# Performance work log

Hardware: AMD Instinct MI355X
Metric: run time of the kernel (lower is better)

The kernel has to match this reference:

```python
import jax, jax.numpy as jnp
import numpy as np


def setup_inputs() -> dict:
    key = jax.random.key(0)
    k1, k2, k3, k4 = jax.random.split(key, 4)
    Q, S, L, F, H = 32, 25, 64, 256, 64
    qs = jax.random.normal(k1, (Q, L, F), dtype=jnp.float32)
    hs = jax.random.normal(k2, (S, L, F), dtype=jnp.float32)
    # nn.Linear(feature_size, hidden_size): weight [H, F], bias [H]
    W = jax.random.normal(k3, (H, F), dtype=jnp.float32) * (1.0 / np.sqrt(F))
    b = jax.random.normal(k4, (H,), dtype=jnp.float32) * 0.01
    return {"qs": qs, "hs": hs, "W": W, "b": b}


def reference(qs, hs, W, b):
    # Project once instead of materializing the repeated 5D tensors before Linear.
    # Wq: [Q, L, H], Wh: [S, L, H]
    Wq = jnp.einsum("qlf,hf->qlh", qs, W) + b
    Wh = jnp.einsum("slf,hf->slh", hs, W) + b
    # score[q,s,i,j] = sum_h tanh(Wq[q,i,h] * Wh[s,j,h])  -- non-decomposable,
    # so the broadcasted [Q,S,L,L,H] tanh is the faithful (and dominant) compute.
    scores = jnp.sum(
        jnp.tanh(Wq[:, None, :, None, :] * Wh[None, :, None, :, :]), axis=-1
    )  # [Q, S, L, L]
    att = jax.nn.softmax(scores, axis=3)  # softmax over support sequence dim j
    # weighted sum of support states: hs_rep[q,s,i,j,:] = hs[s,j,:]
    out = jnp.einsum("qsij,sjf->qsif", att, hs)  # [Q, S, L, F]
    return out
```

## Files before the change

kernel.cpp:

```cpp
#include <hip/hip_runtime.h>


#define NQ 32
#define NS 25
#define NL 64
#define NF 256
#define NH 64

#define K2LOG2E 2.8853900817779268f

typedef __attribute__((ext_vector_type(8))) short bf16x8;
typedef __attribute__((ext_vector_type(4))) float f32x4;
typedef __attribute__((ext_vector_type(2))) float v2f;

__device__ inline unsigned short f2bf(float x) {
    union { float f; unsigned int u; } v; v.f = x;
    unsigned int r = v.u + 0x7fffu + ((v.u >> 16) & 1u);
    return (unsigned short)(r >> 16);
}

__device__ inline void cvt_hilo(float4 a, float4 b, bf16x8* hi, bf16x8* lo) {
    float x[8] = {a.x, a.y, a.z, a.w, b.x, b.y, b.z, b.w};
    bf16x8 h8, l8;
#pragma unroll
    for (int i = 0; i < 8; ++i) {
        union { float f; unsigned int u; } v; v.f = x[i];
        unsigned short hh = (unsigned short)(v.u >> 16);
        h8[i] = (short)hh;
        union { unsigned int u; float f; } hf; hf.u = (unsigned int)hh << 16;
        union { float f; unsigned int u; } rv; rv.f = x[i] - hf.f;
        l8[i] = (short)(unsigned short)(rv.u >> 16);
    }
    *hi = h8; *lo = l8;
}

#define PROJ_BLOCKS 114
__global__ __launch_bounds__(256) void prep_kernel(
    const float* __restrict__ qs, const float* __restrict__ hs,
    const float* __restrict__ W, const float* __restrict__ b,
    float* __restrict__ Wqs, float* __restrict__ Whs,
    unsigned short* __restrict__ hsT)
{
    __shared__ unsigned short T[64 * 72];
    const int t = threadIdx.x;
    const int bid = blockIdx.x;

    if (bid < PROJ_BLOCKS) {
        const int w = t >> 6, lane = t & 63;
        const int m15 = lane & 15, quad = lane >> 4;
        const int r0 = bid * 32 + (w & 1) * 16;
        const int h0 = (w >> 1) * 32;
        const bool is_q = (r0 < 2048);
        const float* Xrow = is_q ? (qs + (size_t)(r0 + m15) * NF)
                                 : (hs + (size_t)(r0 - 2048 + m15) * NF);
        f32x4 acc[2] = {(f32x4){0.f,0.f,0.f,0.f}, (f32x4){0.f,0.f,0.f,0.f}};

#pragma unroll 2
        for (int kk = 0; kk < 8; ++kk) {
            const int f0 = kk * 32 + quad * 8;
            bf16x8 xhi, xlo;
            cvt_hilo(*(const float4*)(Xrow + f0), *(const float4*)(Xrow + f0 + 4),
                     &xhi, &xlo);
#pragma unroll
            for (int nt = 0; nt < 2; ++nt) {
                const float* Wrow = W + (size_t)(h0 + nt * 16 + m15) * NF + f0;
                bf16x8 whi, wlo;
                cvt_hilo(*(const float4*)(Wrow), *(const float4*)(Wrow + 4),
                         &whi, &wlo);
                acc[nt] = __builtin_amdgcn_mfma_f32_16x16x32_bf16(xhi, whi, acc[nt], 0, 0, 0);
                acc[nt] = __builtin_amdgcn_mfma_f32_16x16x32_bf16(xhi, wlo, acc[nt], 0, 0, 0);
                acc[nt] = __builtin_amdgcn_mfma_f32_16x16x32_bf16(xlo, whi, acc[nt], 0, 0, 0);
            }
        }
#pragma unroll
        for (int nt = 0; nt < 2; ++nt) {
            const int h = h0 + nt * 16 + m15;
            const float bias = b[h];
#pragma unroll
            for (int r = 0; r < 4; ++r) {
                const int row = r0 + quad * 4 + r;
                const float v = acc[nt][r] + bias;
                if (is_q) Wqs[(size_t)row * NH + h] = v * K2LOG2E;
                else      Whs[(size_t)(row - 2048) * NH + h] = v;
            }
        }
    } else {
        const int b2 = bid - PROJ_BLOCKS;
        const int s = b2 >> 2;
        const int f0 = (b2 & 3) * 64;
        const float4* h4p = (const float4*)(hs + (size_t)s * NL * NF);
#pragma unroll
        for (int u = 0; u < 4; ++u) {
            int idx = t + 256 * u;
            int j = idx >> 4, fq = idx & 15;
            float4 v = h4p[j * 64 + (f0 >> 2) + fq];
            T[(4 * fq + 0) * 72 + j] = f2bf(v.x);
            T[(4 * fq + 1) * 72 + j] = f2bf(v.y);
            T[(4 * fq + 2) * 72 + j] = f2bf(v.z);
            T[(4 * fq + 3) * 72 + j] = f2bf(v.w);
        }
        __syncthreads();
#pragma unroll
        for (int u = 0; u < 2; ++u) {
            int idx = t + 256 * u;
            int fl = idx >> 3, jg = idx & 7;
            uint4 v = *(const uint4*)&T[fl * 72 + jg * 8];
            *(uint4*)&hsT[(size_t)(s * 256 + f0 + fl) * 64 + jg * 8] = v;
        }
    }
}

__device__ inline void score8(v2f alo, v2f ahi, float4 b0, float4 b1, v2f* sum) {
    const v2f vcl = {30.f, 30.f};
    v2f xlo0 = __builtin_elementwise_min(alo * (v2f){b0.x, b0.y}, vcl);
    v2f xhi0 = __builtin_elementwise_min(ahi * (v2f){b0.z, b0.w}, vcl);
    v2f xlo1 = __builtin_elementwise_min(alo * (v2f){b1.x, b1.y}, vcl);
    v2f xhi1 = __builtin_elementwise_min(ahi * (v2f){b1.z, b1.w}, vcl);
    v2f E0 = { __builtin_amdgcn_exp2f(xlo0[0]), __builtin_amdgcn_exp2f(xlo1[0]) };
    v2f E1 = { __builtin_amdgcn_exp2f(xlo0[1]), __builtin_amdgcn_exp2f(xlo1[1]) };
    v2f E2 = { __builtin_amdgcn_exp2f(xhi0[0]), __builtin_amdgcn_exp2f(xhi1[0]) };
    v2f E3 = { __builtin_amdgcn_exp2f(xhi0[1]), __builtin_amdgcn_exp2f(xhi1[1]) };
    v2f S01 = E0 + E1, S23 = E2 + E3;
    v2f D01 = __builtin_elementwise_fma(E0, E1, S01) + (v2f){1.f, 1.f};
    v2f D23 = __builtin_elementwise_fma(E2, E3, S23) + (v2f){1.f, 1.f};
    v2f U01 = S01 + (v2f){2.f, 2.f};
    v2f U23 = S23 + (v2f){2.f, 2.f};
    v2f NUM = __builtin_elementwise_fma(U01, D23, U23 * D01);
    v2f PROD = D01 * D23;
    v2f R = { __builtin_amdgcn_rcpf(PROD[0]), __builtin_amdgcn_rcpf(PROD[1]) };
    *sum = __builtin_elementwise_fma(NUM, R, *sum);
}

#define AS 68
#define B_OFF 1088
#define SMEMF 5440

__global__ __launch_bounds__(256, 7) void attn_kernel(
    const float* __restrict__ Wqs, const float* __restrict__ Whs,
    const unsigned short* __restrict__ hsT, float* __restrict__ out)
{
    __shared__ float smem[SMEMF];
    const int t = threadIdx.x;
    const int bid = blockIdx.x;
    const int qt = bid & 3;
    const int s = (bid >> 2) % NS;
    const int q = bid / (4 * NS);

    {
        const float4* a4 = (const float4*)(Wqs + ((size_t)q * NL + qt * 16) * NH);
        const float4* b4 = (const float4*)(Whs + (size_t)s * NL * NH);
        {
            int i = t >> 4, g = t & 15;
            *(float4*)&smem[i * AS + 4 * g] = a4[t];
        }
#pragma unroll
        for (int u = 0; u < 4; ++u) {
            int idx = t + 256 * u;
            int j = idx >> 4, g = idx & 15;
            *(float4*)&smem[B_OFF + j * AS + 4 * g] = b4[idx];
        }
    }
    __syncthreads();

    const int irow = t >> 4;
    const int jn = t & 15;
    v2f sumA = {0.f, 0.f}, sumB = {0.f, 0.f};
    {
        const float* Ab = &smem[irow * AS];
        const float* Bb = &smem[B_OFF + jn * AS];

#pragma unroll 4
        for (int h4 = 0; h4 < 16; ++h4) {
            float4 av = *(const float4*)(Ab + 4 * h4);
            v2f alo = {av.x, av.y}, ahi = {av.z, av.w};
            float4 b0 = *(const float4*)(Bb + 4 * h4);
            float4 b1 = *(const float4*)(Bb + 16 * AS + 4 * h4);
            score8(alo, ahi, b0, b1, &sumA);
            float4 b2 = *(const float4*)(Bb + 32 * AS + 4 * h4);
            float4 b3 = *(const float4*)(Bb + 48 * AS + 4 * h4);
            score8(alo, ahi, b2, b3, &sumB);
        }
    }
    __syncthreads();

    {
        float sum[4] = {sumA[0], sumA[1], sumB[0], sumB[1]};
        float mn = fminf(fminf(sum[0], sum[1]), fminf(sum[2], sum[3]));
        mn = fminf(mn, __shfl_xor(mn, 1));
        mn = fminf(mn, __shfl_xor(mn, 2));
        mn = fminf(mn, __shfl_xor(mn, 4));
        mn = fminf(mn, __shfl_xor(mn, 8));
        float p[4];
        float d = 0.f;
#pragma unroll
        for (int jj = 0; jj < 4; ++jj) {
            p[jj] = __builtin_amdgcn_exp2f((mn - sum[jj]) * K2LOG2E);
            d += p[jj];
        }
        d += __shfl_xor(d, 1);
        d += __shfl_xor(d, 2);
        d += __shfl_xor(d, 4);
        d += __shfl_xor(d, 8);
        const float inv = __builtin_amdgcn_rcpf(d);
        unsigned short* att = (unsigned short*)smem;
#pragma unroll
        for (int jj = 0; jj < 4; ++jj)
            att[irow * 72 + jn + 16 * jj] = f2bf(p[jj] * inv);
    }
    __syncthreads();

    const int lane = t & 63;
    const int wv = t >> 6;
    const int m15 = lane & 15;
    const int quad = lane >> 4;

    bf16x8 afr[2];
#pragma unroll
    for (int k = 0; k < 2; ++k)
        afr[k] = *(const bf16x8*)((const char*)smem + m15 * 144 + k * 64 + quad * 16);

    const unsigned short* hsTs = hsT + (size_t)s * NF * NL;
    f32x4 acc[4];
#pragma unroll
    for (int n = 0; n < 4; ++n) acc[n] = (f32x4){0.f, 0.f, 0.f, 0.f};

#pragma unroll
    for (int k = 0; k < 2; ++k) {
        bf16x8 bfr[4];
#pragma unroll
        for (int n = 0; n < 4; ++n)
            bfr[n] = *(const bf16x8*)(hsTs
                        + (size_t)((wv * 4 + n) * 16 + m15) * 64 + k * 32 + quad * 8);
#pragma unroll
        for (int n = 0; n < 4; ++n)
            acc[n] = __builtin_amdgcn_mfma_f32_16x16x32_bf16(afr[k], bfr[n], acc[n], 0, 0, 0);
    }

    const size_t obase = ((size_t)(q * NS + s) * NL + qt * 16) * NF;
#pragma unroll
    for (int n = 0; n < 4; ++n)
#pragma unroll
        for (int r = 0; r < 4; ++r)
            out[obase + (size_t)(quad * 4 + r) * NF + (wv * 4 + n) * 16 + m15] = acc[n][r];
}

extern "C" void kernel_launch(void* const* d_in, const int* in_sizes, int n_in,
                              void* d_out, int out_size, void* d_ws, size_t ws_size,
                              hipStream_t stream) {
    const float* qs = (const float*)d_in[0];
    const float* hs = (const float*)d_in[1];
    const float* W  = (const float*)d_in[2];
    const float* b  = (const float*)d_in[3];
    float* out = (float*)d_out;

    float* Wqs = (float*)d_ws;
    float* Whs = Wqs + NQ * NL * NH;
    unsigned short* hsT = (unsigned short*)(Whs + NS * NL * NH);

    prep_kernel<<<PROJ_BLOCKS + NS * 4, 256, 0, stream>>>(qs, hs, W, b, Wqs, Whs, hsT);
    attn_kernel<<<NQ * NS * 4, 256, 0, stream>>>(Wqs, Whs, hsT, out);
}
```

Baseline: 117.7 us.

## Process 32 query rows per block and software-prefetch score operands

```diff
diff --git a/kernel.cpp b/kernel.cpp
--- a/kernel.cpp
+++ b/kernel.cpp
@@ -132,26 +132,28 @@
 }
 
 #define AS 68
-#define B_OFF 1088
-#define SMEMF 5440
-
-__global__ __launch_bounds__(256, 7) void attn_kernel(
+#define B_OFF 2176
+#define SMEMF 6528
+
+__global__ __launch_bounds__(256, 6) void attn_kernel(
     const float* __restrict__ Wqs, const float* __restrict__ Whs,
     const unsigned short* __restrict__ hsT, float* __restrict__ out)
 {
     __shared__ float smem[SMEMF];
     const int t = threadIdx.x;
     const int bid = blockIdx.x;
-    const int qt = bid & 3;
-    const int s = (bid >> 2) % NS;
-    const int q = bid / (4 * NS);
+    const int qt = bid & 1;
+    const int s = (bid >> 1) % NS;
+    const int q = bid / (2 * NS);
 
     {
-        const float4* a4 = (const float4*)(Wqs + ((size_t)q * NL + qt * 16) * NH);
+        const float4* a4 = (const float4*)(Wqs + ((size_t)q * NL + qt * 32) * NH);
         const float4* b4 = (const float4*)(Whs + (size_t)s * NL * NH);
-        {
-            int i = t >> 4, g = t & 15;
-            *(float4*)&smem[i * AS + 4 * g] = a4[t];
+#pragma unroll
+        for (int u = 0; u < 2; ++u) {
+            int idx = t + 256 * u;
+            int i = idx >> 4, g = idx & 15;
+            *(float4*)&smem[i * AS + 4 * g] = a4[idx];
         }
 #pragma unroll
         for (int u = 0; u < 4; ++u) {
@@ -164,48 +166,81 @@
 
     const int irow = t >> 4;
     const int jn = t & 15;
-    v2f sumA = {0.f, 0.f}, sumB = {0.f, 0.f};
+    v2f s0A = {0.f, 0.f}, s0B = {0.f, 0.f};
+    v2f s1A = {0.f, 0.f}, s1B = {0.f, 0.f};
     {
-        const float* Ab = &smem[irow * AS];
+        const float* A0 = &smem[irow * AS];
+        const float* A1 = &smem[(irow + 16) * AS];
         const float* Bb = &smem[B_OFF + jn * AS];
+
+        float4 av0 = *(const float4*)(A0);
+        float4 av1 = *(const float4*)(A1);
+        float4 bv0 = *(const float4*)(Bb);
+        float4 bv1 = *(const float4*)(Bb + 16 * AS);
+        float4 bv2 = *(const float4*)(Bb + 32 * AS);
+        float4 bv3 = *(const float4*)(Bb + 48 * AS);
 
 #pragma unroll 4
         for (int h4 = 0; h4 < 16; ++h4) {
-            float4 av = *(const float4*)(Ab + 4 * h4);
-            v2f alo = {av.x, av.y}, ahi = {av.z, av.w};
-            float4 b0 = *(const float4*)(Bb + 4 * h4);
-            float4 b1 = *(const float4*)(Bb + 16 * AS + 4 * h4);
-            score8(alo, ahi, b0, b1, &sumA);
-            float4 b2 = *(const float4*)(Bb + 32 * AS + 4 * h4);
-            float4 b3 = *(const float4*)(Bb + 48 * AS + 4 * h4);
-            score8(alo, ahi, b2, b3, &sumB);
+            const int hn = ((h4 + 1) & 15) * 4;
+            float4 na0 = *(const float4*)(A0 + hn);
+            float4 na1 = *(const float4*)(A1 + hn);
+            float4 nb0 = *(const float4*)(Bb + hn);
+            float4 nb1 = *(const float4*)(Bb + 16 * AS + hn);
+            float4 nb2 = *(const float4*)(Bb + 32 * AS + hn);
+            float4 nb3 = *(const float4*)(Bb + 48 * AS + hn);
+
+            v2f a0lo = {av0.x, av0.y}, a0hi = {av0.z, av0.w};
+            v2f a1lo = {av1.x, av1.y}, a1hi = {av1.z, av1.w};
+            score8(a0lo, a0hi, bv0, bv1, &s0A);
+            score8(a0lo, a0hi, bv2, bv3, &s0B);
+            score8(a1lo, a1hi, bv0, bv1, &s1A);
+            score8(a1lo, a1hi, bv2, bv3, &s1B);
+
+            av0 = na0; av1 = na1;
+            bv0 = nb0; bv1 = nb1; bv2 = nb2; bv3 = nb3;
         }
     }
     __syncthreads();
 
     {
-        float sum[4] = {sumA[0], sumA[1], sumB[0], sumB[1]};
-        float mn = fminf(fminf(sum[0], sum[1]), fminf(sum[2], sum[3]));
-        mn = fminf(mn, __shfl_xor(mn, 1));
-        mn = fminf(mn, __shfl_xor(mn, 2));
-        mn = fminf(mn, __shfl_xor(mn, 4));
-        mn = fminf(mn, __shfl_xor(mn, 8));
-        float p[4];
-        float d = 0.f;
+        float sum0[4] = {s0A[0], s0A[1], s0B[0], s0B[1]};
+        float sum1[4] = {s1A[0], s1A[1], s1B[0], s1B[1]};
+        float mn0 = fminf(fminf(sum0[0], sum0[1]), fminf(sum0[2], sum0[3]));
+        float mn1 = fminf(fminf(sum1[0], sum1[1]), fminf(sum1[2], sum1[3]));
+        mn0 = fminf(mn0, __shfl_xor(mn0, 1));
+        mn1 = fminf(mn1, __shfl_xor(mn1, 1));
+        mn0 = fminf(mn0, __shfl_xor(mn0, 2));
+        mn1 = fminf(mn1, __shfl_xor(mn1, 2));
+        mn0 = fminf(mn0, __shfl_xor(mn0, 4));
+        mn1 = fminf(mn1, __shfl_xor(mn1, 4));
+        mn0 = fminf(mn0, __shfl_xor(mn0, 8));
+        mn1 = fminf(mn1, __shfl_xor(mn1, 8));
+        float p0[4], p1[4];
+        float d0 = 0.f, d1 = 0.f;
 #pragma unroll
         for (int jj = 0; jj < 4; ++jj) {
-            p[jj] = __builtin_amdgcn_exp2f((mn - sum[jj]) * K2LOG2E);
-            d += p[jj];
-        }
-        d += __shfl_xor(d, 1);
-        d += __shfl_xor(d, 2);
-        d += __shfl_xor(d, 4);
-        d += __shfl_xor(d, 8);
-        const float inv = __builtin_amdgcn_rcpf(d);
+            p0[jj] = __builtin_amdgcn_exp2f((mn0 - sum0[jj]) * K2LOG2E);
+            p1[jj] = __builtin_amdgcn_exp2f((mn1 - sum1[jj]) * K2LOG2E);
+            d0 += p0[jj];
+            d1 += p1[jj];
+        }
+        d0 += __shfl_xor(d0, 1);
+        d1 += __shfl_xor(d1, 1);
+        d0 += __shfl_xor(d0, 2);
+        d1 += __shfl_xor(d1, 2);
+        d0 += __shfl_xor(d0, 4);
+        d1 += __shfl_xor(d1, 4);
+        d0 += __shfl_xor(d0, 8);
+        d1 += __shfl_xor(d1, 8);
+        const float inv0 = __builtin_amdgcn_rcpf(d0);
+        const float inv1 = __builtin_amdgcn_rcpf(d1);
         unsigned short* att = (unsigned short*)smem;
 #pragma unroll
-        for (int jj = 0; jj < 4; ++jj)
-            att[irow * 72 + jn + 16 * jj] = f2bf(p[jj] * inv);
+        for (int jj = 0; jj < 4; ++jj) {
+            att[irow * 72 + jn + 16 * jj] = f2bf(p0[jj] * inv0);
+            att[(irow + 16) * 72 + jn + 16 * jj] = f2bf(p1[jj] * inv1);
+        }
     }
     __syncthreads();
 
@@ -214,15 +249,20 @@
     const int m15 = lane & 15;
     const int quad = lane >> 4;
 
-    bf16x8 afr[2];
-#pragma unroll
-    for (int k = 0; k < 2; ++k)
-        afr[k] = *(const bf16x8*)((const char*)smem + m15 * 144 + k * 64 + quad * 16);
+    bf16x8 afr[2][2];
+#pragma unroll
+    for (int m = 0; m < 2; ++m)
+#pragma unroll
+        for (int k = 0; k < 2; ++k)
+            afr[m][k] = *(const bf16x8*)((const char*)smem
+                            + (m * 16 + m15) * 144 + k * 64 + quad * 16);
 
     const unsigned short* hsTs = hsT + (size_t)s * NF * NL;
-    f32x4 acc[4];
-#pragma unroll
-    for (int n = 0; n < 4; ++n) acc[n] = (f32x4){0.f, 0.f, 0.f, 0.f};
+    f32x4 acc[2][4];
+#pragma unroll
+    for (int m = 0; m < 2; ++m)
+#pragma unroll
+        for (int n = 0; n < 4; ++n) acc[m][n] = (f32x4){0.f, 0.f, 0.f, 0.f};
 
 #pragma unroll
     for (int k = 0; k < 2; ++k) {
@@ -232,16 +272,21 @@
             bfr[n] = *(const bf16x8*)(hsTs
                         + (size_t)((wv * 4 + n) * 16 + m15) * 64 + k * 32 + quad * 8);
 #pragma unroll
+        for (int n = 0; n < 4; ++n) {
+            acc[0][n] = __builtin_amdgcn_mfma_f32_16x16x32_bf16(afr[0][k], bfr[n], acc[0][n], 0, 0, 0);
+            acc[1][n] = __builtin_amdgcn_mfma_f32_16x16x32_bf16(afr[1][k], bfr[n], acc[1][n], 0, 0, 0);
+        }
+    }
+
+    const size_t obase = ((size_t)(q * NS + s) * NL + qt * 32) * NF;
+#pragma unroll
+    for (int m = 0; m < 2; ++m)
+#pragma unroll
         for (int n = 0; n < 4; ++n)
-            acc[n] = __builtin_amdgcn_mfma_f32_16x16x32_bf16(afr[k], bfr[n], acc[n], 0, 0, 0);
-    }
-
-    const size_t obase = ((size_t)(q * NS + s) * NL + qt * 16) * NF;
-#pragma unroll
-    for (int n = 0; n < 4; ++n)
-#pragma unroll
-        for (int r = 0; r < 4; ++r)
-            out[obase + (size_t)(quad * 4 + r) * NF + (wv * 4 + n) * 16 + m15] = acc[n][r];
+#pragma unroll
+            for (int r = 0; r < 4; ++r)
+                out[obase + (size_t)(m * 16 + quad * 4 + r) * NF
+                    + (wv * 4 + n) * 16 + m15] = acc[m][n][r];
 }
 
 extern "C" void kernel_launch(void* const* d_in, const int* in_sizes, int n_in,
@@ -258,5 +303,5 @@
     unsigned short* hsT = (unsigned short*)(Whs + NS * NL * NH);
 
     prep_kernel<<<PROJ_BLOCKS + NS * 4, 256, 0, stream>>>(qs, hs, W, b, Wqs, Whs, hsT);
-    attn_kernel<<<NQ * NS * 4, 256, 0, stream>>>(Wqs, Whs, hsT, out);
-}
+    attn_kernel<<<NQ * NS * 2, 256, 0, stream>>>(Wqs, Whs, hsT, out);
+}
```

Result: slower. 120.3 us (+2.1%).

## Process full 64x64 score tile per block with register-held query rows

Applied to the files above, without the earlier changes.

```diff
diff --git a/kernel.cpp b/kernel.cpp
--- a/kernel.cpp
+++ b/kernel.cpp
@@ -131,117 +131,135 @@
     *sum = __builtin_elementwise_fma(NUM, R, *sum);
 }
 
-#define AS 68
-#define B_OFF 1088
-#define SMEMF 5440
-
-__global__ __launch_bounds__(256, 7) void attn_kernel(
+#define SC_S 68
+#define ATT_F 4352
+
+__global__ __launch_bounds__(256, 4) void attn_kernel(
     const float* __restrict__ Wqs, const float* __restrict__ Whs,
     const unsigned short* __restrict__ hsT, float* __restrict__ out)
 {
-    __shared__ float smem[SMEMF];
+    __shared__ float smem[6656];
     const int t = threadIdx.x;
     const int bid = blockIdx.x;
-    const int qt = bid & 3;
-    const int s = (bid >> 2) % NS;
-    const int q = bid / (4 * NS);
-
+    const int s = bid % NS;
+    const int q = bid / NS;
+    const int lane = t & 63;
+    const int wv = t >> 6;
+    const int wvu = __builtin_amdgcn_readfirstlane(wv);
+
+    v2f a2[32];
     {
-        const float4* a4 = (const float4*)(Wqs + ((size_t)q * NL + qt * 16) * NH);
-        const float4* b4 = (const float4*)(Whs + (size_t)s * NL * NH);
-        {
-            int i = t >> 4, g = t & 15;
-            *(float4*)&smem[i * AS + 4 * g] = a4[t];
-        }
-#pragma unroll
-        for (int u = 0; u < 4; ++u) {
-            int idx = t + 256 * u;
-            int j = idx >> 4, g = idx & 15;
-            *(float4*)&smem[B_OFF + j * AS + 4 * g] = b4[idx];
+        const float4* arow = (const float4*)(Wqs + ((size_t)q * NL + lane) * NH);
+#pragma unroll
+        for (int k = 0; k < 16; ++k) {
+            float4 v = arow[k];
+            a2[2 * k]     = (v2f){v.x, v.y};
+            a2[2 * k + 1] = (v2f){v.z, v.w};
+        }
+    }
+
+    {
+        const float* Bb = Whs + ((size_t)s * NL + wvu * 16) * NH;
+#pragma unroll 2
+        for (int jp = 0; jp < 8; ++jp) {
+            const float* bj0 = Bb + jp * NH;
+            const float* bj1 = Bb + (jp + 8) * NH;
+            v2f sum = {0.f, 0.f};
+#pragma unroll
+            for (int h4 = 0; h4 < 16; ++h4) {
+                float4 b0 = *(const float4*)(bj0 + 4 * h4);
+                float4 b1 = *(const float4*)(bj1 + 4 * h4);
+                score8(a2[2 * h4], a2[2 * h4 + 1], b0, b1, &sum);
+            }
+            smem[lane * SC_S + wvu * 16 + jp]     = sum[0];
+            smem[lane * SC_S + wvu * 16 + jp + 8] = sum[1];
         }
     }
     __syncthreads();
 
-    const int irow = t >> 4;
-    const int jn = t & 15;
-    v2f sumA = {0.f, 0.f}, sumB = {0.f, 0.f};
     {
-        const float* Ab = &smem[irow * AS];
-        const float* Bb = &smem[B_OFF + jn * AS];
-
-#pragma unroll 4
-        for (int h4 = 0; h4 < 16; ++h4) {
-            float4 av = *(const float4*)(Ab + 4 * h4);
-            v2f alo = {av.x, av.y}, ahi = {av.z, av.w};
-            float4 b0 = *(const float4*)(Bb + 4 * h4);
-            float4 b1 = *(const float4*)(Bb + 16 * AS + 4 * h4);
-            score8(alo, ahi, b0, b1, &sumA);
-            float4 b2 = *(const float4*)(Bb + 32 * AS + 4 * h4);
-            float4 b3 = *(const float4*)(Bb + 48 * AS + 4 * h4);
-            score8(alo, ahi, b2, b3, &sumB);
-        }
-    }
-    __syncthreads();
-
-    {
-        float sum[4] = {sumA[0], sumA[1], sumB[0], sumB[1]};
-        float mn = fminf(fminf(sum[0], sum[1]), fminf(sum[2], sum[3]));
+        const int si = t >> 2;
+        const int g = t & 3;
+        const float* srow = &smem[si * SC_S + g * 16];
+        float4 s0 = *(const float4*)(srow);
+        float4 s1 = *(const float4*)(srow + 4);
+        float4 s2 = *(const float4*)(srow + 8);
+        float4 s3 = *(const float4*)(srow + 12);
+        float sc[16] = {s0.x, s0.y, s0.z, s0.w, s1.x, s1.y, s1.z, s1.w,
+                        s2.x, s2.y, s2.z, s2.w, s3.x, s3.y, s3.z, s3.w};
+        float mn = sc[0];
+#pragma unroll
+        for (int k = 1; k < 16; ++k) mn = fminf(mn, sc[k]);
         mn = fminf(mn, __shfl_xor(mn, 1));
         mn = fminf(mn, __shfl_xor(mn, 2));
-        mn = fminf(mn, __shfl_xor(mn, 4));
-        mn = fminf(mn, __shfl_xor(mn, 8));
-        float p[4];
+        float p[16];
         float d = 0.f;
 #pragma unroll
-        for (int jj = 0; jj < 4; ++jj) {
-            p[jj] = __builtin_amdgcn_exp2f((mn - sum[jj]) * K2LOG2E);
-            d += p[jj];
+        for (int k = 0; k < 16; ++k) {
+            p[k] = __builtin_amdgcn_exp2f((mn - sc[k]) * K2LOG2E);
+            d += p[k];
         }
         d += __shfl_xor(d, 1);
         d += __shfl_xor(d, 2);
-        d += __shfl_xor(d, 4);
-        d += __shfl_xor(d, 8);
         const float inv = __builtin_amdgcn_rcpf(d);
-        unsigned short* att = (unsigned short*)smem;
-#pragma unroll
-        for (int jj = 0; jj < 4; ++jj)
-            att[irow * 72 + jn + 16 * jj] = f2bf(p[jj] * inv);
+        unsigned int w[8];
+#pragma unroll
+        for (int k = 0; k < 8; ++k)
+            w[k] = (unsigned int)f2bf(p[2 * k] * inv)
+                 | ((unsigned int)f2bf(p[2 * k + 1] * inv) << 16);
+        unsigned short* att = (unsigned short*)(smem + ATT_F);
+        *(uint4*)&att[si * 72 + g * 16]     = (uint4){w[0], w[1], w[2], w[3]};
+        *(uint4*)&att[si * 72 + g * 16 + 8] = (uint4){w[4], w[5], w[6], w[7]};
     }
     __syncthreads();
 
-    const int lane = t & 63;
-    const int wv = t >> 6;
     const int m15 = lane & 15;
     const int quad = lane >> 4;
-
-    bf16x8 afr[2];
-#pragma unroll
-    for (int k = 0; k < 2; ++k)
-        afr[k] = *(const bf16x8*)((const char*)smem + m15 * 144 + k * 64 + quad * 16);
+    const unsigned short* attc = (const unsigned short*)(smem + ATT_F);
+
+    bf16x8 afr[4][2];
+#pragma unroll
+    for (int m = 0; m < 4; ++m)
+#pragma unroll
+        for (int k = 0; k < 2; ++k)
+            afr[m][k] = *(const bf16x8*)((const char*)attc
+                            + (m * 16 + m15) * 144 + k * 64 + quad * 16);
 
     const unsigned short* hsTs = hsT + (size_t)s * NF * NL;
-    f32x4 acc[4];
-#pragma unroll
-    for (int n = 0; n < 4; ++n) acc[n] = (f32x4){0.f, 0.f, 0.f, 0.f};
-
-#pragma unroll
-    for (int k = 0; k < 2; ++k) {
-        bf16x8 bfr[4];
-#pragma unroll
-        for (int n = 0; n < 4; ++n)
-            bfr[n] = *(const bf16x8*)(hsTs
-                        + (size_t)((wv * 4 + n) * 16 + m15) * 64 + k * 32 + quad * 8);
-#pragma unroll
-        for (int n = 0; n < 4; ++n)
-            acc[n] = __builtin_amdgcn_mfma_f32_16x16x32_bf16(afr[k], bfr[n], acc[n], 0, 0, 0);
-    }
-
-    const size_t obase = ((size_t)(q * NS + s) * NL + qt * 16) * NF;
-#pragma unroll
-    for (int n = 0; n < 4; ++n)
-#pragma unroll
-        for (int r = 0; r < 4; ++r)
-            out[obase + (size_t)(quad * 4 + r) * NF + (wv * 4 + n) * 16 + m15] = acc[n][r];
+    const size_t obase = (size_t)(q * NS + s) * NL * NF;
+
+#pragma unroll
+    for (int nh = 0; nh < 2; ++nh) {
+        f32x4 acc[4][2];
+#pragma unroll
+        for (int m = 0; m < 4; ++m)
+#pragma unroll
+            for (int n = 0; n < 2; ++n) acc[m][n] = (f32x4){0.f, 0.f, 0.f, 0.f};
+
+#pragma unroll
+        for (int k = 0; k < 2; ++k) {
+            bf16x8 bfr[2];
+#pragma unroll
+            for (int n = 0; n < 2; ++n)
+                bfr[n] = *(const bf16x8*)(hsTs
+                            + (size_t)((wv * 4 + nh * 2 + n) * 16 + m15) * 64
+                            + k * 32 + quad * 8);
+#pragma unroll
+            for (int n = 0; n < 2; ++n)
+#pragma unroll
+                for (int m = 0; m < 4; ++m)
+                    acc[m][n] = __builtin_amdgcn_mfma_f32_16x16x32_bf16(
+                        afr[m][k], bfr[n], acc[m][n], 0, 0, 0);
+        }
+#pragma unroll
+        for (int m = 0; m < 4; ++m)
+#pragma unroll
+            for (int n = 0; n < 2; ++n)
+#pragma unroll
+                for (int r = 0; r < 4; ++r)
+                    out[obase + (size_t)(m * 16 + quad * 4 + r) * NF
+                        + (wv * 4 + nh * 2 + n) * 16 + m15] = acc[m][n][r];
+    }
 }
 
 extern "C" void kernel_launch(void* const* d_in, const int* in_sizes, int n_in,
@@ -258,5 +276,5 @@
     unsigned short* hsT = (unsigned short*)(Whs + NS * NL * NH);
 
     prep_kernel<<<PROJ_BLOCKS + NS * 4, 256, 0, stream>>>(qs, hs, W, b, Wqs, Whs, hsT);
-    attn_kernel<<<NQ * NS * 4, 256, 0, stream>>>(Wqs, Whs, hsT, out);
-}
+    attn_kernel<<<NQ * NS, 256, 0, stream>>>(Wqs, Whs, hsT, out);
+}
```

Result: slower. 131.8 us (+12.0%).
